# Kernel optimization log

Measured on AMD Instinct MI355X. Metric: run time of the kernel, lower is better.

Reference implementation:

```python
import jax, jax.numpy as jnp
import numpy as np
from jax import lax


def setup_inputs() -> dict:
    key = jax.random.key(0)
    k1, k2 = jax.random.split(key)
    B, T, H, L = 64, 512, 768, 400
    hidden_states = jax.random.normal(k1, (B, T, H), dtype=jnp.float32)
    text_labels_length = jax.random.randint(k2, (B,), 1, L, dtype=jnp.int32)
    return {
        "hidden_states": hidden_states,
        "text_labels_length": text_labels_length,
        "max_label_length": L,  # static python int (min(max(lengths), 400))
    }


def reference(hidden_states, text_labels_length, max_label_length):
    # hidden_states: [B, T, H]; last channel is the CIF firing weight alpha.
    B, T, H = hidden_states.shape
    L = int(max_label_length)
    dtype = hidden_states.dtype

    alpha = jax.nn.sigmoid(hidden_states[:, :, -1])                 # [B, T]
    lengths = jnp.minimum(text_labels_length, L).astype(dtype)      # clamp to max_label_length
    alpha_sum = alpha.sum(axis=1)                                   # [B]
    scale = lengths / alpha_sum
    alpha_p = alpha * scale[:, None]                                # [B, T]
    hs = hidden_states[:, :, :-1]                                   # [B, T, H-1]

    # scan over the first L timesteps (original loops k in range(max_label_length))
    a_seq = jnp.swapaxes(alpha_p[:, :L], 0, 1)                      # [L, B]
    h_seq = jnp.swapaxes(hs[:, :L], 0, 1)                           # [L, B, H-1]

    def step(carry, xs):
        a_r, s_r = carry                                            # [B], [B, H-1]
        ak, hk = xs                                                 # [B], [B, H-1]
        a_a = ak + a_r
        fired = a_a >= 1.0
        # accumulation weight this step: full alpha if not fired, else residual (1 - a_r)
        w = jnp.where(fired, 1.0 - a_r, ak)                         # [B]
        s_a_k = s_r + w[:, None] * hk                               # [B, H-1]
        a_r_new = jnp.where(fired, ak - (1.0 - a_r), a_a)           # [B]
        s_r_new = jnp.where(fired[:, None], a_r_new[:, None] * hk, s_a_k)
        return (a_r_new, s_r_new), s_a_k

    init = (jnp.zeros((B,), dtype), jnp.zeros((B, H - 1), dtype))
    _, s_a = lax.scan(step, init, (a_seq, h_seq))                   # [L, B, H-1]
    s_a = jnp.swapaxes(s_a, 0, 1)                                   # [B, L, H-1]

    n_hat = ((lengths - alpha_sum) ** 2).sum()
    return s_a, n_hat
```

## Files before the change

### kernel.cpp

```cpp
#include <hip/hip_runtime.h>
#include <math.h>

namespace {
constexpr int kB  = 64;
constexpr int kT  = 512;
constexpr int kH  = 768;
constexpr int kHm = 767;
constexpr int kL  = 400;
}

__device__ __forceinline__ float sigmoidf_(float x) {
  return 1.0f / (1.0f + expf(-x));
}

__global__ __launch_bounds__(512) void k_rec(
    const float* __restrict__ hs, const int* __restrict__ labels,
    float* __restrict__ asum_ws, float4* __restrict__ wms) {
  __shared__ float a_lds[kT];
  __shared__ float red[kT];
  const int b = blockIdx.x;
  const int tid = threadIdx.x;

  float sig = sigmoidf_(hs[(size_t)b * kT * kH + (size_t)tid * kH + kHm]);
  a_lds[tid] = sig;
  red[tid] = sig;
  __syncthreads();
  for (int off = 256; off > 0; off >>= 1) {
    if (tid < off) red[tid] += red[tid + off];
    __syncthreads();
  }

  if (tid == 0) {
    const float as = red[0];
    asum_ws[b] = as;
    const int lab = labels[b];
    const float len = (float)(lab < kL ? lab : kL);
    const float scale = len / as;
    float a_r = 0.0f;
    float4* wb = wms + b * kL;
#pragma unroll 8
    for (int k = 0; k < kL; ++k) {
      const float ak = a_lds[k] * scale;
      const float a_a = ak + a_r;
      const bool fired = (a_a >= 1.0f);
      const float w   = fired ? (1.0f - a_r) : ak;
      const float arn = fired ? (ak - (1.0f - a_r)) : a_a;
      const float m   = fired ? arn : ak;
      const float sel = fired ? 0.0f : 1.0f;
      wb[k] = make_float4(w, m, sel, 0.0f);
      a_r = arn;
    }
  }
}

__global__ __launch_bounds__(256) void k_scan(
    const float* __restrict__ hs, const int* __restrict__ labels,
    const float* __restrict__ asum_ws, const float4* __restrict__ wms,
    float* __restrict__ out) {
  __shared__ float4 lw[kL];
  const int b = blockIdx.y;
  const int tid = threadIdx.x;

  for (int i = tid; i < kL; i += 256) lw[i] = wms[b * kL + i];
  __syncthreads();

  if (blockIdx.x == 0 && b == 0 && tid < kB) {
    const float as = asum_ws[tid];
    const int lab = labels[tid];
    const float len = (float)(lab < kL ? lab : kL);
    float d = len - as;
    float v = d * d;
    for (int off = 32; off > 0; off >>= 1) v += __shfl_down(v, off, 64);
    if (tid == 0) out[(size_t)kB * kL * kHm] = v;
  }

  const int h = blockIdx.x * 256 + tid;
  if (h >= kHm) return;

  const float* __restrict__ px = hs + (size_t)b * kT * kH + h;
  float* __restrict__ po = out + (size_t)b * kL * kHm + h;
  float s = 0.0f;
#pragma unroll 8
  for (int k = 0; k < kL; ++k) {
    const float x = px[(size_t)k * kH];
    const float4 c = lw[k];
    const float o = fmaf(c.x, x, s);
    po[(size_t)k * kHm] = o;
    s = fmaf(c.y, x, c.z * s);
  }
}

extern "C" void kernel_launch(void* const* d_in, const int* in_sizes, int n_in,
                              void* d_out, int out_size, void* d_ws, size_t ws_size,
                              hipStream_t stream) {
  const float* hs     = (const float*)d_in[0];
  const int*   labels = (const int*)d_in[1];
  float* out = (float*)d_out;

  float*  asum_ws = (float*)d_ws;
  float4* wms     = (float4*)((char*)d_ws + 256);

  k_rec<<<kB, 512, 0, stream>>>(hs, labels, asum_ws, wms);
  k_scan<<<dim3((kHm + 255) / 256, kB), 256, 0, stream>>>(hs, labels, asum_ws,
                                                          wms, out);
}
```

Before: 49.97 us.

## Double-buffer scan loads in register blocks to overlap memory with compute

The per-column scan in k_scan now loads 40 timesteps of hidden states into a register array while computing the previous block, ping-ponging two buffers across the 400 steps. This is meant to hide global-load latency behind the serial FMA chain by keeping many loads in flight. The recurrence kernel's unroll factor is also raised from 8 to 16. The added 80 registers per thread may lower occupancy or cause spills.

```diff
diff --git a/kernel.cpp b/kernel.cpp
--- a/kernel.cpp
+++ b/kernel.cpp
@@ -7,6 +7,7 @@
 constexpr int kH  = 768;
 constexpr int kHm = 767;
 constexpr int kL  = 400;
+constexpr int kBK = 40;
 }
 
 __device__ __forceinline__ float sigmoidf_(float x) {
@@ -38,7 +39,7 @@
     const float scale = len / as;
     float a_r = 0.0f;
     float4* wb = wms + b * kL;
-#pragma unroll 8
+#pragma unroll 16
     for (int k = 0; k < kL; ++k) {
       const float ak = a_lds[k] * scale;
       const float a_a = ak + a_r;
@@ -50,6 +51,24 @@
       wb[k] = make_float4(w, m, sel, 0.0f);
       a_r = arn;
     }
+  }
+}
+
+__device__ __forceinline__ void load_blk(const float* __restrict__ px, int k0,
+                                         float (&x)[kBK]) {
+#pragma unroll
+  for (int i = 0; i < kBK; ++i) x[i] = px[(size_t)(k0 + i) * kH];
+}
+
+__device__ __forceinline__ void comp_blk(const float4* __restrict__ lw,
+                                         float* __restrict__ po, int k0,
+                                         const float (&x)[kBK], float& s) {
+#pragma unroll
+  for (int i = 0; i < kBK; ++i) {
+    const float4 c = lw[k0 + i];
+    const float o = fmaf(c.x, x[i], s);
+    po[(size_t)(k0 + i) * kHm] = o;
+    s = fmaf(c.y, x[i], c.z * s);
   }
 }
 
@@ -79,14 +98,16 @@
 
   const float* __restrict__ px = hs + (size_t)b * kT * kH + h;
   float* __restrict__ po = out + (size_t)b * kL * kHm + h;
+
+  float xa[kBK], xb[kBK];
   float s = 0.0f;
-#pragma unroll 8
-  for (int k = 0; k < kL; ++k) {
-    const float x = px[(size_t)k * kH];
-    const float4 c = lw[k];
-    const float o = fmaf(c.x, x, s);
-    po[(size_t)k * kHm] = o;
-    s = fmaf(c.y, x, c.z * s);
+  load_blk(px, 0, xa);
+  for (int sb = 0; sb < 5; ++sb) {
+    const int k0 = sb * 2 * kBK;
+    load_blk(px, k0 + kBK, xb);
+    comp_blk(lw, po, k0, xa, s);
+    if (sb < 4) load_blk(px, k0 + 2 * kBK, xa);
+    comp_blk(lw, po, k0 + kBK, xb, s);
   }
 }
 
```

Result: faster. 47.47 us (-5.0%).

## Split CIF scan into fire-delimited segments processed by independent blocks

Applied to the files above, without the earlier changes.

The recurrence kernel now records, for each of 16 fixed chunks of the label axis, the step just after the last firing before that chunk. Because the accumulated state resets at every firing to depend only on that step's input, each segment between these start points can be scanned on its own. The scan kernel gains a third grid dimension so each segment runs in a separate block, which raises parallelism from one serial 400-step loop per block. It also batches 32 strided loads ahead of the dependent FMA chain to hide memory latency. Load balance depends on how often firings occur: a batch with few firings leaves one long segment, and empty segments launch blocks that exit immediately.

```diff
diff --git a/kernel.cpp b/kernel.cpp
--- a/kernel.cpp
+++ b/kernel.cpp
@@ -7,6 +7,10 @@
 constexpr int kH  = 768;
 constexpr int kHm = 767;
 constexpr int kL  = 400;
+constexpr int kC  = 16;
+constexpr int kTC = kL / kC;
+constexpr int kBK = 32;
+constexpr int kLwPad = kL + kBK;
 }
 
 __device__ __forceinline__ float sigmoidf_(float x) {
@@ -15,7 +19,8 @@
 
 __global__ __launch_bounds__(512) void k_rec(
     const float* __restrict__ hs, const int* __restrict__ labels,
-    float* __restrict__ asum_ws, float4* __restrict__ wms) {
+    float* __restrict__ asum_ws, int* __restrict__ starts_ws,
+    float4* __restrict__ wms) {
   __shared__ float a_lds[kT];
   __shared__ float red[kT];
   const int b = blockIdx.x;
@@ -37,56 +42,85 @@
     const float len = (float)(lab < kL ? lab : kL);
     const float scale = len / as;
     float a_r = 0.0f;
+    int last_fire = -1;
     float4* wb = wms + b * kL;
-#pragma unroll 8
-    for (int k = 0; k < kL; ++k) {
-      const float ak = a_lds[k] * scale;
-      const float a_a = ak + a_r;
-      const bool fired = (a_a >= 1.0f);
-      const float w   = fired ? (1.0f - a_r) : ak;
-      const float arn = fired ? (ak - (1.0f - a_r)) : a_a;
-      const float m   = fired ? arn : ak;
-      const float sel = fired ? 0.0f : 1.0f;
-      wb[k] = make_float4(w, m, sel, 0.0f);
-      a_r = arn;
+    int* sb = starts_ws + b * (kC + 1);
+    for (int c = 0; c < kC; ++c) {
+      sb[c] = last_fire + 1;
+      const int kbase = c * kTC;
+#pragma unroll
+      for (int kk = 0; kk < kTC; ++kk) {
+        const int k = kbase + kk;
+        const float ak = a_lds[k] * scale;
+        const float a_a = ak + a_r;
+        const bool fired = (a_a >= 1.0f);
+        const float w   = fired ? (1.0f - a_r) : ak;
+        const float arn = fired ? (ak - (1.0f - a_r)) : a_a;
+        const float m   = fired ? arn : ak;
+        const float sel = fired ? 0.0f : 1.0f;
+        wb[k] = make_float4(w, m, sel, 0.0f);
+        if (fired) last_fire = k;
+        a_r = arn;
+      }
     }
+    sb[kC] = kL;
   }
 }
 
 __global__ __launch_bounds__(256) void k_scan(
     const float* __restrict__ hs, const int* __restrict__ labels,
-    const float* __restrict__ asum_ws, const float4* __restrict__ wms,
-    float* __restrict__ out) {
-  __shared__ float4 lw[kL];
+    const float* __restrict__ asum_ws, const int* __restrict__ starts_ws,
+    const float4* __restrict__ wms, float* __restrict__ out) {
+  __shared__ float4 lw[kLwPad];
   const int b = blockIdx.y;
+  const int c = blockIdx.z;
   const int tid = threadIdx.x;
 
   for (int i = tid; i < kL; i += 256) lw[i] = wms[b * kL + i];
-  __syncthreads();
+  for (int i = kL + tid; i < kLwPad; i += 256) lw[i] = make_float4(0, 0, 0, 0);
 
-  if (blockIdx.x == 0 && b == 0 && tid < kB) {
+  if (blockIdx.x == 0 && b == 0 && c == 0 && tid < kB) {
     const float as = asum_ws[tid];
     const int lab = labels[tid];
     const float len = (float)(lab < kL ? lab : kL);
-    float d = len - as;
+    const float d = len - as;
     float v = d * d;
     for (int off = 32; off > 0; off >>= 1) v += __shfl_down(v, off, 64);
     if (tid == 0) out[(size_t)kB * kL * kHm] = v;
   }
+  __syncthreads();
+
+  const int start = __builtin_amdgcn_readfirstlane(starts_ws[b * (kC + 1) + c]);
+  const int end   = __builtin_amdgcn_readfirstlane(starts_ws[b * (kC + 1) + c + 1]);
+  if (start >= end) return;
 
   const int h = blockIdx.x * 256 + tid;
   if (h >= kHm) return;
 
   const float* __restrict__ px = hs + (size_t)b * kT * kH + h;
   float* __restrict__ po = out + (size_t)b * kL * kHm + h;
+
   float s = 0.0f;
-#pragma unroll 8
-  for (int k = 0; k < kL; ++k) {
-    const float x = px[(size_t)k * kH];
-    const float4 c = lw[k];
-    const float o = fmaf(c.x, x, s);
-    po[(size_t)k * kHm] = o;
-    s = fmaf(c.y, x, c.z * s);
+  if (start > 0) {
+    const float xj = px[(size_t)(start - 1) * kH];
+    s = lw[start - 1].y * xj;
+  }
+
+  for (int k0 = start; k0 < end; k0 += kBK) {
+    float x[kBK];
+#pragma unroll
+    for (int i = 0; i < kBK; ++i) {
+      x[i] = px[(size_t)(k0 + i) * kH];
+    }
+#pragma unroll
+    for (int i = 0; i < kBK; ++i) {
+      const float4 c4 = lw[k0 + i];
+      if (k0 + i < end) {
+        const float o = fmaf(c4.x, x[i], s);
+        po[(size_t)(k0 + i) * kHm] = o;
+        s = fmaf(c4.y, x[i], c4.z * s);
+      }
+    }
   }
 }
 
@@ -97,10 +131,11 @@
   const int*   labels = (const int*)d_in[1];
   float* out = (float*)d_out;
 
-  float*  asum_ws = (float*)d_ws;
-  float4* wms     = (float4*)((char*)d_ws + 256);
+  float*  asum_ws   = (float*)d_ws;
+  int*    starts_ws = (int*)((char*)d_ws + 256);
+  float4* wms       = (float4*)((char*)d_ws + 8192);
 
-  k_rec<<<kB, 512, 0, stream>>>(hs, labels, asum_ws, wms);
-  k_scan<<<dim3((kHm + 255) / 256, kB), 256, 0, stream>>>(hs, labels, asum_ws,
-                                                          wms, out);
+  k_rec<<<kB, 512, 0, stream>>>(hs, labels, asum_ws, starts_ws, wms);
+  k_scan<<<dim3((kHm + 255) / 256, kB, kC), 256, 0, stream>>>(
+      hs, labels, asum_ws, starts_ws, wms, out);
 }
```

Result: slower. 75.95 us (+52.0%).

## Split time scan into chunks with fire-reset carry propagation and float4 loads

Applied to the files above, without the earlier changes.

The 400-step recurrence is split into 8 time chunks. A new pass computes each chunk's partial carry, starting from its last firing step. The main scan then seeds each chunk by summing partial carries from the last chunk that fired, which exposes parallelism over time. The hidden dimension is also processed four channels per thread with float4 loads. The cost is an extra kernel launch and extra re-reads of the input for the carry pass. The carry composition relies on the fire reset removing earlier history, and ordering of floating-point adds may change.

```diff
diff --git a/kernel.cpp b/kernel.cpp
--- a/kernel.cpp
+++ b/kernel.cpp
@@ -5,8 +5,12 @@
 constexpr int kB  = 64;
 constexpr int kT  = 512;
 constexpr int kH  = 768;
+constexpr int kH4 = kH / 4;
 constexpr int kHm = 767;
 constexpr int kL  = 400;
+constexpr int kC  = 8;
+constexpr int kTC = kL / kC;
+constexpr int kTh = 192;
 }
 
 __device__ __forceinline__ float sigmoidf_(float x) {
@@ -15,7 +19,8 @@
 
 __global__ __launch_bounds__(512) void k_rec(
     const float* __restrict__ hs, const int* __restrict__ labels,
-    float* __restrict__ asum_ws, float4* __restrict__ wms) {
+    float* __restrict__ asum_ws, int* __restrict__ rstart_ws,
+    int* __restrict__ cstart_ws, float4* __restrict__ wms) {
   __shared__ float a_lds[kT];
   __shared__ float red[kT];
   const int b = blockIdx.x;
@@ -37,56 +42,117 @@
     const float len = (float)(lab < kL ? lab : kL);
     const float scale = len / as;
     float a_r = 0.0f;
+    int lfc = -1;
     float4* wb = wms + b * kL;
-#pragma unroll 8
-    for (int k = 0; k < kL; ++k) {
-      const float ak = a_lds[k] * scale;
-      const float a_a = ak + a_r;
-      const bool fired = (a_a >= 1.0f);
-      const float w   = fired ? (1.0f - a_r) : ak;
-      const float arn = fired ? (ak - (1.0f - a_r)) : a_a;
-      const float m   = fired ? arn : ak;
-      const float sel = fired ? 0.0f : 1.0f;
-      wb[k] = make_float4(w, m, sel, 0.0f);
-      a_r = arn;
+    for (int c = 0; c < kC; ++c) {
+      cstart_ws[b * kC + c] = lfc < 0 ? 0 : lfc;
+      int lf = -1;
+      const int kbase = c * kTC;
+#pragma unroll
+      for (int kk = 0; kk < kTC; ++kk) {
+        const int k = kbase + kk;
+        const float ak = a_lds[k] * scale;
+        const float a_a = ak + a_r;
+        const bool fired = (a_a >= 1.0f);
+        const float w   = fired ? (1.0f - a_r) : ak;
+        const float arn = fired ? (ak - (1.0f - a_r)) : a_a;
+        const float m   = fired ? arn : ak;
+        const float sel = fired ? 0.0f : 1.0f;
+        wb[k] = make_float4(w, m, sel, 0.0f);
+        if (fired) lf = k;
+        a_r = arn;
+      }
+      rstart_ws[b * kC + c] = lf >= 0 ? lf : kbase;
+      if (lf >= 0) lfc = c;
     }
   }
 }
 
-__global__ __launch_bounds__(256) void k_scan(
+__global__ __launch_bounds__(kTh) void k_q(
     const float* __restrict__ hs, const int* __restrict__ labels,
-    const float* __restrict__ asum_ws, const float4* __restrict__ wms,
+    const float* __restrict__ asum_ws, const int* __restrict__ rstart_ws,
+    const float4* __restrict__ wms, float4* __restrict__ q_ws,
     float* __restrict__ out) {
   __shared__ float4 lw[kL];
-  const int b = blockIdx.y;
-  const int tid = threadIdx.x;
+  const int b = blockIdx.x, c = blockIdx.y, tid = threadIdx.x;
 
-  for (int i = tid; i < kL; i += 256) lw[i] = wms[b * kL + i];
-  __syncthreads();
+  for (int i = tid; i < kL; i += kTh) lw[i] = wms[b * kL + i];
 
-  if (blockIdx.x == 0 && b == 0 && tid < kB) {
+  if (b == 0 && c == 0 && tid < kB) {
     const float as = asum_ws[tid];
     const int lab = labels[tid];
     const float len = (float)(lab < kL ? lab : kL);
-    float d = len - as;
+    const float d = len - as;
     float v = d * d;
     for (int off = 32; off > 0; off >>= 1) v += __shfl_down(v, off, 64);
     if (tid == 0) out[(size_t)kB * kL * kHm] = v;
   }
+  __syncthreads();
 
-  const int h = blockIdx.x * 256 + tid;
-  if (h >= kHm) return;
+  const int r1 = __builtin_amdgcn_readfirstlane(rstart_ws[b * kC + c]);
+  const int ce = c * kTC + kTC;
+  const float4* __restrict__ px = (const float4*)(hs + (size_t)b * kT * kH) + tid;
 
-  const float* __restrict__ px = hs + (size_t)b * kT * kH + h;
-  float* __restrict__ po = out + (size_t)b * kL * kHm + h;
-  float s = 0.0f;
-#pragma unroll 8
-  for (int k = 0; k < kL; ++k) {
-    const float x = px[(size_t)k * kH];
-    const float4 c = lw[k];
-    const float o = fmaf(c.x, x, s);
-    po[(size_t)k * kHm] = o;
-    s = fmaf(c.y, x, c.z * s);
+  float4 s = make_float4(0.f, 0.f, 0.f, 0.f);
+#pragma unroll 5
+  for (int k = r1; k < ce; ++k) {
+    const float4 x = px[(size_t)k * kH4];
+    const float4 cf = lw[k];
+    s.x = fmaf(cf.y, x.x, cf.z * s.x);
+    s.y = fmaf(cf.y, x.y, cf.z * s.y);
+    s.z = fmaf(cf.y, x.z, cf.z * s.z);
+    s.w = fmaf(cf.y, x.w, cf.z * s.w);
+  }
+  q_ws[(size_t)(b * kC + c) * kH4 + tid] = s;
+}
+
+__global__ __launch_bounds__(kTh) void k_scan(
+    const float* __restrict__ hs, const int* __restrict__ cstart_ws,
+    const float4* __restrict__ wms, const float4* __restrict__ q_ws,
+    float* __restrict__ out) {
+  __shared__ float4 lw[kL];
+  const int b = blockIdx.x, c = blockIdx.y, tid = threadIdx.x;
+
+  for (int i = tid; i < kL; i += kTh) lw[i] = wms[b * kL + i];
+  __syncthreads();
+
+  const int cs = __builtin_amdgcn_readfirstlane(cstart_ws[b * kC + c]);
+
+  float4 s = make_float4(0.f, 0.f, 0.f, 0.f);
+  {
+    const float4* qb = q_ws + (size_t)b * kC * kH4 + tid;
+    float4 qv[kC - 1];
+#pragma unroll
+    for (int j = 0; j < kC - 1; ++j) qv[j] = qb[(size_t)j * kH4];
+#pragma unroll
+    for (int j = 0; j < kC - 1; ++j) {
+      if (j >= cs && j < c) {
+        s.x += qv[j].x; s.y += qv[j].y; s.z += qv[j].z; s.w += qv[j].w;
+      }
+    }
+  }
+
+  const int cb = c * kTC, ce = cb + kTC;
+  const float4* __restrict__ px = (const float4*)(hs + (size_t)b * kT * kH) + tid;
+  const int h0 = 4 * tid;
+  float* __restrict__ po = out + (size_t)b * kL * kHm + h0;
+  const bool w3 = (h0 + 3 < kHm);
+
+#pragma unroll 10
+  for (int k = cb; k < ce; ++k) {
+    const float4 x = px[(size_t)k * kH4];
+    const float4 cf = lw[k];
+    const float o0 = fmaf(cf.x, x.x, s.x);
+    const float o1 = fmaf(cf.x, x.y, s.y);
+    const float o2 = fmaf(cf.x, x.z, s.z);
+    const float o3 = fmaf(cf.x, x.w, s.w);
+    float* r = po + (size_t)k * kHm;
+    r[0] = o0; r[1] = o1; r[2] = o2;
+    if (w3) r[3] = o3;
+    s.x = fmaf(cf.y, x.x, cf.z * s.x);
+    s.y = fmaf(cf.y, x.y, cf.z * s.y);
+    s.z = fmaf(cf.y, x.z, cf.z * s.z);
+    s.w = fmaf(cf.y, x.w, cf.z * s.w);
   }
 }
 
@@ -97,10 +163,14 @@
   const int*   labels = (const int*)d_in[1];
   float* out = (float*)d_out;
 
-  float*  asum_ws = (float*)d_ws;
-  float4* wms     = (float4*)((char*)d_ws + 256);
+  float*  asum_ws   = (float*)d_ws;
+  int*    rstart_ws = (int*)((char*)d_ws + 256);
+  int*    cstart_ws = (int*)((char*)d_ws + 2304);
+  float4* wms       = (float4*)((char*)d_ws + 8192);
+  float4* q_ws      = (float4*)((char*)d_ws + (512 << 10));
 
-  k_rec<<<kB, 512, 0, stream>>>(hs, labels, asum_ws, wms);
-  k_scan<<<dim3((kHm + 255) / 256, kB), 256, 0, stream>>>(hs, labels, asum_ws,
-                                                          wms, out);
+  k_rec<<<kB, 512, 0, stream>>>(hs, labels, asum_ws, rstart_ws, cstart_ws, wms);
+  k_q<<<dim3(kB, kC), kTh, 0, stream>>>(hs, labels, asum_ws, rstart_ws, wms,
+                                        q_ws, out);
+  k_scan<<<dim3(kB, kC), kTh, 0, stream>>>(hs, cstart_ws, wms, q_ws, out);
 }
```

Result: slower. 56.84 us (+13.7%).
